# Kernel tuning notes

Measured on AMD Instinct MI355X. Metric: run time of the kernel, lower is better.

Reference implementation:

```python
import jax, jax.numpy as jnp
import numpy as np

NUM_HEADS = 16

def setup_inputs() -> dict:
    key = jax.random.key(0)
    ks = jax.random.split(key, 7)
    B, Q, K, D = 4, 512, 4096, 1024
    return {
        'query':  jax.random.normal(ks[0], (B, Q, D), dtype=jnp.float32),
        'memory': jax.random.normal(ks[1], (B, K, D), dtype=jnp.float32),
        'bias':   jax.random.normal(ks[2], (B, K), dtype=jnp.float32),
        'Wq': jax.random.normal(ks[3], (D, D), dtype=jnp.float32) * (D ** -0.5),
        'Wk': jax.random.normal(ks[4], (D, D), dtype=jnp.float32) * (D ** -0.5),
        'Wv': jax.random.normal(ks[5], (D, D), dtype=jnp.float32) * (D ** -0.5),
        'Wo': jax.random.normal(ks[6], (D, D), dtype=jnp.float32) * (D ** -0.5),
    }

def reference(query, memory, bias, Wq, Wk, Wv, Wo):
    B, Qn, _ = query.shape
    _, Kn, _ = memory.shape
    H = NUM_HEADS
    E = Wq.shape[1]
    dh = E // H
    scale = dh ** -0.5
    # projections (bias-free linears), split heads: [B, H, len, dh]
    q = (query @ Wq).reshape(B, Qn, H, dh).transpose(0, 2, 1, 3)
    k = (memory @ Wk).reshape(B, Kn, H, dh).transpose(0, 2, 1, 3)
    v = (memory @ Wv).reshape(B, Kn, H, dh).transpose(0, 2, 1, 3)
    scores = jnp.einsum('bhqd,bhkd->bhqk', q, k) * scale
    scores = scores + bias[:, None, None, :]          # additive support bias over K
    weights = jax.nn.softmax(scores, axis=-1)          # dropout p=0.0 -> identity
    out = jnp.einsum('bhqk,bhkd->bhqd', weights, v)
    out = out.transpose(0, 2, 1, 3).reshape(B, Qn, E)
    return out @ Wo
```

## Files before the change

kernel.cpp:

```cpp
#include <hip/hip_runtime.h>

typedef __attribute__((ext_vector_type(8))) short bf16x8;
typedef __attribute__((ext_vector_type(4))) short bf16x4;
typedef __attribute__((ext_vector_type(4))) float f32x4;

#define MFMA32(a,b,c) __builtin_amdgcn_mfma_f32_16x16x32_bf16((a),(b),(c),0,0,0)
#define MFMA16(a,b,c) __builtin_amdgcn_mfma_f32_16x16x16bf16_1k((a),(b),(c),0,0,0)
#define LOG2E 1.44269504f

#define BAR() asm volatile("s_barrier" ::: "memory")
#define VMW(n) asm volatile("s_waitcnt vmcnt(" #n ")" ::: "memory")

__device__ __forceinline__ unsigned short f2bf(float f) {
  unsigned int u = __float_as_uint(f);
  u += 0x7fffu + ((u >> 16) & 1u);
  return (unsigned short)(u >> 16);
}

__device__ __forceinline__ void cp16(const void* g, void* l) {
  __builtin_amdgcn_global_load_lds((const __attribute__((address_space(1))) void*)g,
                                   (__attribute__((address_space(3))) void*)l, 16, 0, 0);
}

__global__ void conv_both(const float* __restrict__ q, const float* __restrict__ m,
                          const float* __restrict__ bias,
                          unsigned short* __restrict__ qo, unsigned short* __restrict__ mo,
                          float* __restrict__ bz) {
  int i = blockIdx.x * 256 + threadIdx.x;
  if (i < 524288) {
    float4 v = ((const float4*)q)[i];
    ushort4 o; o.x = f2bf(v.x); o.y = f2bf(v.y); o.z = f2bf(v.z); o.w = f2bf(v.w);
    ((ushort4*)qo)[i] = o;
  } else if (i < 4718592) {
    int j = i - 524288;
    float4 v = ((const float4*)m)[j];
    ushort4 o; o.x = f2bf(v.x); o.y = f2bf(v.y); o.z = f2bf(v.z); o.w = f2bf(v.w);
    ((ushort4*)mo)[j] = o;
  } else {
    int j = i - 4718592;
    float4 v = ((const float4*)bias)[j];
    float4 o;
    o.x = __builtin_fmaf(v.x, LOG2E, -16.f);
    o.y = __builtin_fmaf(v.y, LOG2E, -16.f);
    o.z = __builtin_fmaf(v.z, LOG2E, -16.f);
    o.w = __builtin_fmaf(v.w, LOG2E, -16.f);
    ((float4*)bz)[j] = o;
  }
}

__global__ void transpose4(const float* __restrict__ Wq, const float* __restrict__ Wk,
                           const float* __restrict__ Wv, const float* __restrict__ Wo,
                           unsigned short* __restrict__ dst) {
  __shared__ float t[32][33];
  int z = blockIdx.z;
  const float* W = (z == 0) ? Wq : (z == 1) ? Wk : (z == 2) ? Wv : Wo;
  unsigned short* WT = dst + (size_t)z * 1048576;
  int bx = blockIdx.x * 32, by = blockIdx.y * 32;
  int x = threadIdx.x, y0 = threadIdx.y;
#pragma unroll
  for (int r = 0; r < 4; ++r)
    t[y0 + r * 8][x] = W[(size_t)(by + y0 + r * 8) * 1024 + bx + x];
  __syncthreads();
#pragma unroll
  for (int r = 0; r < 4; ++r)
    WT[(size_t)(bx + y0 + r * 8) * 1024 + by + x] = f2bf(t[x][y0 + r * 8]);
}

__global__ __launch_bounds__(512, 2) void gemm_kv(
    const unsigned short* __restrict__ A,
    const unsigned short* __restrict__ Bk,
    const unsigned short* __restrict__ Bv,
    unsigned short* __restrict__ Kp,
    unsigned short* __restrict__ Vt)
{
  __shared__ __attribute__((aligned(16))) unsigned short lds[65536];
  const int tid = threadIdx.x;
  const int w = tid >> 6, lane = tid & 63;
  const int lh = lane & 15, q4 = lane >> 4;
  const int id = blockIdx.x;
  const int xcd = id & 7, j = id >> 3;
  const int tm = (xcd * 8 + (j >> 3)) * 256;
  const int tn = (j & 7) * 128;
  const int wm = (w >> 1) * 64, wn = (w & 1) * 64;

  const int r8 = lane >> 3;
  const int scol = ((lane & 7) ^ r8) * 8;
  const int srow = w * 8 + r8;
  const int fs0 = ((0 + q4) ^ (lh & 7)) * 8;
  const int fs1 = ((4 + q4) ^ (lh & 7)) * 8;

  const unsigned short* Ag = A  + (size_t)tm * 1024 + scol;
  const unsigned short* Kg = Bk + (size_t)tn * 1024 + scol;
  const unsigned short* Vg = Bv + (size_t)tn * 1024 + scol;

#define STG_A(BUF,KT,I) cp16(Ag + (size_t)((I)*64 + srow) * 1024 + (KT)*64, \
                             lds + (BUF)*32768 + (I)*4096 + w*512)
#define STG_K(BUF,KT,I) cp16(Kg + (size_t)((I)*64 + srow) * 1024 + (KT)*64, \
                             lds + (BUF)*32768 + 16384 + (I)*4096 + w*512)
#define STG_V(BUF,KT,I) cp16(Vg + (size_t)((I)*64 + srow) * 1024 + (KT)*64, \
                             lds + (BUF)*32768 + 24576 + (I)*4096 + w*512)

  f32x4 acck[4][4] = {}, accv[4][4] = {};

  STG_A(0, 0, 0); STG_A(0, 0, 1); STG_A(0, 0, 2); STG_A(0, 0, 3);
  STG_K(0, 0, 0); STG_K(0, 0, 1);
  STG_V(0, 0, 0); STG_V(0, 0, 1);
  STG_A(1, 1, 0); STG_A(1, 1, 1); STG_A(1, 1, 2); STG_A(1, 1, 3);
  VMW(6);
  BAR();

#define KV_TILE(CURB, TP1, TP2, DO_SB, DO_SA, VM1N, DO_V3, VM3N)              \
  {                                                                           \
    const unsigned short* bse = lds + (CURB) * 32768;                         \
    const int nx = (CURB) ^ 1;                                                \
    bf16x8 a0[4], a1[4], bfr[4];                                              \
                                                  \
    _Pragma("unroll") for (int m = 0; m < 4; ++m)                             \
      a0[m] = *(const bf16x8*)(bse + (wm + m * 16 + lh) * 64 + fs0);          \
    _Pragma("unroll") for (int n = 0; n < 4; ++n)                             \
      bfr[n] = *(const bf16x8*)(bse + 16384 + (wn + n * 16 + lh) * 64 + fs0); \
    if (DO_SB) { STG_K(nx, TP1, 0); STG_K(nx, TP1, 1); }                      \
    BAR();                                                                    \
    __builtin_amdgcn_s_setprio(1);                                            \
    _Pragma("unroll") for (int m = 0; m < 4; ++m)                             \
      _Pragma("unroll") for (int n = 0; n < 4; ++n)                           \
        acck[m][n] = MFMA32(a0[m], bfr[n], acck[m][n]);                       \
    __builtin_amdgcn_s_setprio(0);                                            \
    BAR();                                                                    \
                                                  \
    _Pragma("unroll") for (int m = 0; m < 4; ++m)                             \
      a1[m] = *(const bf16x8*)(bse + (wm + m * 16 + lh) * 64 + fs1);          \
    _Pragma("unroll") for (int n = 0; n < 4; ++n)                             \
      bfr[n] = *(const bf16x8*)(bse + 16384 + (wn + n * 16 + lh) * 64 + fs1); \
    if (DO_SB) { STG_V(nx, TP1, 0); STG_V(nx, TP1, 1); }                      \
    BAR();                                                                    \
    __builtin_amdgcn_s_setprio(1);                                            \
    _Pragma("unroll") for (int m = 0; m < 4; ++m)                             \
      _Pragma("unroll") for (int n = 0; n < 4; ++n)                           \
        acck[m][n] = MFMA32(a1[m], bfr[n], acck[m][n]);                       \
    __builtin_amdgcn_s_setprio(0);                                            \
    VMW(VM1N);                                                                \
    BAR();                                                                    \
                                  \
    _Pragma("unroll") for (int n = 0; n < 4; ++n)                             \
      bfr[n] = *(const bf16x8*)(bse + 24576 + (wn + n * 16 + lh) * 64 + fs0); \
    if (DO_SA) { STG_A(CURB, TP2, 0); STG_A(CURB, TP2, 1); }                  \
    BAR();                                                                    \
    __builtin_amdgcn_s_setprio(1);                                            \
    _Pragma("unroll") for (int m = 0; m < 4; ++m)                             \
      _Pragma("unroll") for (int n = 0; n < 4; ++n)                           \
        accv[m][n] = MFMA32(a0[m], bfr[n], accv[m][n]);                       \
    __builtin_amdgcn_s_setprio(0);                                            \
    BAR();                                                                    \
                                                  \
    _Pragma("unroll") for (int n = 0; n < 4; ++n)                             \
      bfr[n] = *(const bf16x8*)(bse + 24576 + (wn + n * 16 + lh) * 64 + fs1); \
    if (DO_SA) { STG_A(CURB, TP2, 2); STG_A(CURB, TP2, 3); }                  \
    BAR();                                                                    \
    __builtin_amdgcn_s_setprio(1);                                            \
    _Pragma("unroll") for (int m = 0; m < 4; ++m)                             \
      _Pragma("unroll") for (int n = 0; n < 4; ++n)                           \
        accv[m][n] = MFMA32(a1[m], bfr[n], accv[m][n]);                       \
    __builtin_amdgcn_s_setprio(0);                                            \
    if (DO_V3) { VMW(VM3N); }                                                 \
    BAR();                                                                    \
  }

  for (int t = 0; t < 14; ++t) {
    KV_TILE(t & 1, t + 1, t + 2, 1, 1, 8, 1, 6);
  }
  KV_TILE(0, 15, 16, 1, 0, 8, 1, 2);
  KV_TILE(1, 16, 17, 0, 0, 0, 0, 0);

#undef KV_TILE
#undef STG_A
#undef STG_K
#undef STG_V

#pragma unroll
  for (int m = 0; m < 4; ++m)
#pragma unroll
    for (int n = 0; n < 4; ++n) {
      int row = tm + wm + m * 16 + q4 * 4;
      int col = tn + wn + n * 16 + lh;
#pragma unroll
      for (int e = 0; e < 4; ++e)
        Kp[(size_t)(row + e) * 1024 + col] = f2bf(acck[m][n][e]);
    }

#pragma unroll
  for (int m = 0; m < 4; ++m)
#pragma unroll
    for (int n = 0; n < 4; ++n) {
      int row = wm + m * 16 + q4 * 4;
      int col = wn + n * 16 + lh;
      ushort4 v4;
      v4.x = f2bf(accv[m][n][0]); v4.y = f2bf(accv[m][n][1]);
      v4.z = f2bf(accv[m][n][2]); v4.w = f2bf(accv[m][n][3]);
      *(ushort4*)(lds + col * 256 + (row ^ ((col & 31) << 3))) = v4;
    }
  __syncthreads();
#pragma unroll
  for (int p = 0; p < 8; ++p) {
    int col = p * 16 + (tid >> 5);
    int jb = tid & 31;
    const unsigned short* src = lds + col * 256 + ((jb ^ (col & 31)) << 3);
    *(int4*)(Vt + (size_t)(tn + col) * 16384 + tm + jb * 8) = *(const int4*)src;
  }
}

__global__ __launch_bounds__(256) void gemm_bt64(
    const unsigned short* __restrict__ A, const unsigned short* __restrict__ B,
    float* __restrict__ Cf, unsigned short* __restrict__ Cb,
    int M, int N, int K, float scale)
{
  __shared__ __attribute__((aligned(16))) unsigned short lds[6144];
  int w = threadIdx.x >> 6, lane = threadIdx.x & 63;
  int lh = lane & 15, q4 = lane >> 4;
  int tm = blockIdx.y * 128, tn = blockIdx.x * 64;
  int wm = (w & 1) * 64, wn = (w >> 1) * 32;

  int srow = lane >> 2;
  int scol = ((lane & 3) ^ ((lane >> 3) & 3)) << 3;
  int q4s = (q4 ^ ((lh >> 1) & 3)) << 3;

  f32x4 acc[4][2] = {};

  for (int k0 = 0; k0 < K; k0 += 32) {
#pragma unroll
    for (int i = 0; i < 2; ++i) {
      int c = w * 2 + i;
      int row = c * 16 + srow;
      cp16(A + (size_t)(tm + row) * K + k0 + scol, lds + c * 512);
    }
    {
      int row = w * 16 + srow;
      cp16(B + (size_t)(tn + row) * K + k0 + scol, lds + 4096 + w * 512);
    }
    __syncthreads();
    bf16x8 afr[4], bfr[2];
#pragma unroll
    for (int r = 0; r < 4; ++r)
      afr[r] = *(const bf16x8*)(lds + (wm + r * 16 + lh) * 32 + q4s);
#pragma unroll
    for (int c = 0; c < 2; ++c)
      bfr[c] = *(const bf16x8*)(lds + 4096 + (wn + c * 16 + lh) * 32 + q4s);
#pragma unroll
    for (int r = 0; r < 4; ++r)
#pragma unroll
      for (int c = 0; c < 2; ++c)
        acc[r][c] = MFMA32(afr[r], bfr[c], acc[r][c]);
    __syncthreads();
  }

#pragma unroll
  for (int r = 0; r < 4; ++r)
#pragma unroll
    for (int c = 0; c < 2; ++c)
#pragma unroll
      for (int e = 0; e < 4; ++e) {
        int row = tm + wm + r * 16 + q4 * 4 + e;
        int col = tn + wn + c * 16 + lh;
        if (Cb) Cb[(size_t)row * N + col] = f2bf(acc[r][c][e] * scale);
        else    Cf[(size_t)row * N + col] = acc[r][c][e] * scale;
      }
}

__global__ __launch_bounds__(256) void attn_kernel(
    const unsigned short* __restrict__ Q, const unsigned short* __restrict__ Kp,
    const unsigned short* __restrict__ VT, const float* __restrict__ bz,
    float* __restrict__ po, float* __restrict__ lp)
{
  __shared__ __attribute__((aligned(16))) unsigned short Klds[4096];
  __shared__ __attribute__((aligned(16))) unsigned short Vlds[4096];
  int w = threadIdx.x >> 6, lane = threadIdx.x & 63;
  int lh = lane & 15, q4 = lane >> 4;

  int id = blockIdx.x;
  int xcd = id & 7, j = id >> 3;
  int ql = j & 7;
  int half = ql & 1, qt = ql >> 1;
  int bh = (j >> 3) * 8 + xcd;
  int b = bh >> 4, h = bh & 15;
  int q0 = qt * 128;
  int t00 = half * 2048;

  const unsigned short* Qb = Q + (size_t)(b * 512 + q0 + w * 32) * 1024 + h * 64;
  const unsigned short* Kb = Kp + (size_t)(b * 4096) * 1024 + h * 64;
  const unsigned short* Vb = VT + (size_t)(h * 64) * 16384 + b * 4096;
  const float* bzg = bz + (size_t)b * 4096;

  bf16x8 bq[2][2];
#pragma unroll
  for (int s = 0; s < 2; ++s)
#pragma unroll
    for (int th = 0; th < 2; ++th)
      bq[s][th] = *(const bf16x8*)(Qb + (size_t)(s * 16 + lh) * 1024 + th * 32 + q4 * 8);

  f32x4 oa[2][4] = {};
  float ls[2] = {0.f, 0.f};

  int rl = lane >> 3, blk = lane & 7;
  int sw = ((blk ^ rl) * 8);

  for (int ti = 0; ti < 32; ++ti) {
    int t = t00 + ti * 64;
#pragma unroll
    for (int r = 0; r < 2; ++r) {
      int seg = r * 4 + w;
      int row = seg * 8 + rl;
      cp16(Kb + (size_t)(t + row) * 1024 + sw, Klds + seg * 512);
      cp16(Vb + (size_t)row * 16384 + t + sw, Vlds + seg * 512);
    }
    __syncthreads();

    float4 bz4[4];
#pragma unroll
    for (int c = 0; c < 4; ++c)
      bz4[c] = *(const float4*)(bzg + t + c * 16 + q4 * 4);

    bf16x8 kf[4][2];
#pragma unroll
    for (int c = 0; c < 4; ++c)
#pragma unroll
      for (int th = 0; th < 2; ++th)
        kf[c][th] = *(const bf16x8*)(Klds + (c * 16 + lh) * 64 + (((th << 2) + q4) ^ (lh & 7)) * 8);
    bf16x4 vf[4][4];
#pragma unroll
    for (int c = 0; c < 4; ++c)
#pragma unroll
      for (int c2 = 0; c2 < 4; ++c2)
        vf[c][c2] = *(const bf16x4*)(Vlds + (c2 * 16 + lh) * 64 +
                                     (((c << 1) + (q4 >> 1)) ^ (lh & 7)) * 8 + (q4 & 1) * 4);

#pragma unroll
    for (int s = 0; s < 2; ++s) {
#pragma unroll
      for (int c = 0; c < 4; ++c) {
        f32x4 z = {};
        z = MFMA32(kf[c][0], bq[s][0], z);
        z = MFMA32(kf[c][1], bq[s][1], z);
        float bzf[4] = {bz4[c].x, bz4[c].y, bz4[c].z, bz4[c].w};
        bf16x4 pb;
        float ps = 0.f;
#pragma unroll
        for (int e = 0; e < 4; ++e) {
          float p = __builtin_amdgcn_exp2f(z[e] + bzf[e]);
          ps += p;
          pb[e] = (short)f2bf(p);
        }
        ls[s] += ps;
#pragma unroll
        for (int c2 = 0; c2 < 4; ++c2)
          oa[s][c2] = MFMA16(vf[c][c2], pb, oa[s][c2]);
      }
    }
    __syncthreads();
  }

#pragma unroll
  for (int s = 0; s < 2; ++s) {
    ls[s] += __shfl_xor(ls[s], 16);
    ls[s] += __shfl_xor(ls[s], 32);
  }

  int sl = bh * 4 + qt;
  float* pslice = po + (size_t)(half * 256 + sl) * 8192;
#pragma unroll
  for (int s = 0; s < 2; ++s) {
    if (q4 == 0) lp[half * 32768 + sl * 128 + w * 32 + s * 16 + lh] = ls[s];
#pragma unroll
    for (int c2 = 0; c2 < 4; ++c2)
#pragma unroll
      for (int e = 0; e < 4; ++e)
        pslice[(c2 * 16 + q4 * 4 + e) * 128 + w * 32 + s * 16 + lh] = oa[s][c2][e];
  }
}

__global__ void norm_kernel(const float* __restrict__ po, const float* __restrict__ lp,
                            unsigned short* __restrict__ ao) {
  int g = blockIdx.x * 256 + threadIdx.x;
  int d8 = (g & 7) * 8;
  int rowid = g >> 3;
  int bh = rowid >> 9, rq = rowid & 511, qt = rq >> 7, qcol = rq & 127;
  int sl = bh * 4 + qt;
  const float* p0 = po + (size_t)sl * 8192;
  const float* p1 = po + (size_t)(256 + sl) * 8192;
  float l = lp[sl * 128 + qcol] + lp[32768 + sl * 128 + qcol];
  float inv = 1.f / l;
  unsigned short o8[8];
#pragma unroll
  for (int k = 0; k < 8; ++k)
    o8[k] = f2bf((p0[(d8 + k) * 128 + qcol] + p1[(d8 + k) * 128 + qcol]) * inv);
  int b = bh >> 4, h = bh & 15;
  unsigned short* dst = ao + (size_t)(b * 512 + qt * 128 + qcol) * 1024 + h * 64 + d8;
  *(ushort4*)dst = *(ushort4*)o8;
  *(ushort4*)(dst + 4) = *(ushort4*)(o8 + 4);
}

extern "C" void kernel_launch(void* const* d_in, const int* in_sizes, int n_in,
                              void* d_out, int out_size, void* d_ws, size_t ws_size,
                              hipStream_t stream) {
  const float* query  = (const float*)d_in[0];
  const float* memory = (const float*)d_in[1];
  const float* bias   = (const float*)d_in[2];
  const float* Wq     = (const float*)d_in[3];
  const float* Wk     = (const float*)d_in[4];
  const float* Wv     = (const float*)d_in[5];
  const float* Wo     = (const float*)d_in[6];
  float* out = (float*)d_out;

  unsigned short* ws  = (unsigned short*)d_ws;
  unsigned short* qbf = ws;
  unsigned short* mbf = qbf + 2097152;
  unsigned short* WqT = mbf + 16777216;
  unsigned short* WkT = WqT + 1048576;
  unsigned short* WvT = WkT + 1048576;
  unsigned short* WoT = WvT + 1048576;
  unsigned short* qp  = WoT + 1048576;
  unsigned short* kp  = qp + 2097152;
  unsigned short* vT  = kp + 16777216;
  unsigned short* ao  = vT + 16777216;
  float* bzw = (float*)(ao + 2097152);
  float* po = (float*)ws;
  float* lp = po + 4194304;

  conv_both<<<18448, 256, 0, stream>>>(query, memory, bias, qbf, mbf, bzw);
  transpose4<<<dim3(32, 32, 4), dim3(32, 8), 0, stream>>>(Wq, Wk, Wv, Wo, WqT);

  gemm_bt64<<<dim3(16, 16), 256, 0, stream>>>(qbf, WqT, nullptr, qp, 2048, 1024, 1024, 0.125f * LOG2E);
  gemm_kv<<<512, 512, 0, stream>>>(mbf, WkT, WvT, kp, vT);

  attn_kernel<<<512, 256, 0, stream>>>(qp, kp, vT, bzw, po, lp);
  norm_kernel<<<1024, 256, 0, stream>>>(po, lp, ao);

  gemm_bt64<<<dim3(16, 16), 256, 0, stream>>>(ao, WoT, out, nullptr, 2048, 1024, 1024, 1.f);
}
```

Measured before the change: 299.3 us.

## Software-pipeline LDS fragment reads with double-buffered registers in KV projection

Restructures the K/V projection tile loop so LDS fragment reads for the next phase (and the next tile's first A/K fragments) are issued before the current MFMA block, using separate register sets instead of reloading each phase. Barriers drop from two per phase to one, and the vmcnt wait thresholds are retuned to fit the new ordering. The aim is to hide LDS read latency behind MFMA work and cut barrier stalls. In exchange it raises register pressure and makes the barrier and wait ordering more fragile, so a read could race with an async LDS fill if a count is wrong. A __syncthreads is added before the V tile is staged into LDS for the transpose.

```diff
diff --git a/kernel.cpp b/kernel.cpp
--- a/kernel.cpp
+++ b/kernel.cpp
@@ -9,7 +9,8 @@
 #define LOG2E 1.44269504f
 
 #define BAR() asm volatile("s_barrier" ::: "memory")
-#define VMW(n) asm volatile("s_waitcnt vmcnt(" #n ")" ::: "memory")
+#define VMW_(n) asm volatile("s_waitcnt vmcnt(" #n ")" ::: "memory")
+#define VMW(n) VMW_(n)
 
 __device__ __forceinline__ unsigned short f2bf(float f) {
   unsigned int u = __float_as_uint(f);
@@ -101,6 +102,7 @@
                              lds + (BUF)*32768 + 24576 + (I)*4096 + w*512)
 
   f32x4 acck[4][4] = {}, accv[4][4] = {};
+  bf16x8 aE[4], aO[4], bP[4], bQ[4];
 
   STG_A(0, 0, 0); STG_A(0, 0, 1); STG_A(0, 0, 2); STG_A(0, 0, 3);
   STG_K(0, 0, 0); STG_K(0, 0, 1);
@@ -108,69 +110,73 @@
   STG_A(1, 1, 0); STG_A(1, 1, 1); STG_A(1, 1, 2); STG_A(1, 1, 3);
   VMW(6);
   BAR();
-
-#define KV_TILE(CURB, TP1, TP2, DO_SB, DO_SA, VM1N, DO_V3, VM3N)              \
+#pragma unroll
+  for (int m = 0; m < 4; ++m)
+    aE[m] = *(const bf16x8*)(lds + (wm + m * 16 + lh) * 64 + fs0);
+#pragma unroll
+  for (int n = 0; n < 4; ++n)
+    bP[n] = *(const bf16x8*)(lds + 16384 + (wn + n * 16 + lh) * 64 + fs0);
+
+#define KV_TILE(CURB, TP1, TP2, DO_SB, DO_SA, VM1N, VM3N, DO_V3, DO_RDN)      \
   {                                                                           \
     const unsigned short* bse = lds + (CURB) * 32768;                         \
+    const unsigned short* bnx = lds + ((CURB) ^ 1) * 32768;                   \
     const int nx = (CURB) ^ 1;                                                \
-    bf16x8 a0[4], a1[4], bfr[4];                                              \
-                                                  \
+                            \
+    BAR();                                                                    \
     _Pragma("unroll") for (int m = 0; m < 4; ++m)                             \
-      a0[m] = *(const bf16x8*)(bse + (wm + m * 16 + lh) * 64 + fs0);          \
+      aO[m] = *(const bf16x8*)(bse + (wm + m * 16 + lh) * 64 + fs1);          \
     _Pragma("unroll") for (int n = 0; n < 4; ++n)                             \
-      bfr[n] = *(const bf16x8*)(bse + 16384 + (wn + n * 16 + lh) * 64 + fs0); \
+      bQ[n] = *(const bf16x8*)(bse + 16384 + (wn + n * 16 + lh) * 64 + fs1);  \
     if (DO_SB) { STG_K(nx, TP1, 0); STG_K(nx, TP1, 1); }                      \
-    BAR();                                                                    \
     __builtin_amdgcn_s_setprio(1);                                            \
     _Pragma("unroll") for (int m = 0; m < 4; ++m)                             \
       _Pragma("unroll") for (int n = 0; n < 4; ++n)                           \
-        acck[m][n] = MFMA32(a0[m], bfr[n], acck[m][n]);                       \
+        acck[m][n] = MFMA32(aE[m], bP[n], acck[m][n]);                        \
     __builtin_amdgcn_s_setprio(0);                                            \
+                      \
+    VMW(VM1N);                                                                \
     BAR();                                                                    \
-                                                  \
-    _Pragma("unroll") for (int m = 0; m < 4; ++m)                             \
-      a1[m] = *(const bf16x8*)(bse + (wm + m * 16 + lh) * 64 + fs1);          \
     _Pragma("unroll") for (int n = 0; n < 4; ++n)                             \
-      bfr[n] = *(const bf16x8*)(bse + 16384 + (wn + n * 16 + lh) * 64 + fs1); \
+      bP[n] = *(const bf16x8*)(bse + 24576 + (wn + n * 16 + lh) * 64 + fs0);  \
     if (DO_SB) { STG_V(nx, TP1, 0); STG_V(nx, TP1, 1); }                      \
-    BAR();                                                                    \
     __builtin_amdgcn_s_setprio(1);                                            \
     _Pragma("unroll") for (int m = 0; m < 4; ++m)                             \
       _Pragma("unroll") for (int n = 0; n < 4; ++n)                           \
-        acck[m][n] = MFMA32(a1[m], bfr[n], acck[m][n]);                       \
+        acck[m][n] = MFMA32(aO[m], bQ[n], acck[m][n]);                        \
     __builtin_amdgcn_s_setprio(0);                                            \
-    VMW(VM1N);                                                                \
+                         \
     BAR();                                                                    \
-                                  \
     _Pragma("unroll") for (int n = 0; n < 4; ++n)                             \
-      bfr[n] = *(const bf16x8*)(bse + 24576 + (wn + n * 16 + lh) * 64 + fs0); \
+      bQ[n] = *(const bf16x8*)(bse + 24576 + (wn + n * 16 + lh) * 64 + fs1);  \
     if (DO_SA) { STG_A(CURB, TP2, 0); STG_A(CURB, TP2, 1); }                  \
-    BAR();                                                                    \
     __builtin_amdgcn_s_setprio(1);                                            \
     _Pragma("unroll") for (int m = 0; m < 4; ++m)                             \
       _Pragma("unroll") for (int n = 0; n < 4; ++n)                           \
-        accv[m][n] = MFMA32(a0[m], bfr[n], accv[m][n]);                       \
+        accv[m][n] = MFMA32(aE[m], bP[n], accv[m][n]);                        \
     __builtin_amdgcn_s_setprio(0);                                            \
+                   \
+    if (DO_V3) { VMW(VM3N); }                                                 \
     BAR();                                                                    \
-                                                  \
-    _Pragma("unroll") for (int n = 0; n < 4; ++n)                             \
-      bfr[n] = *(const bf16x8*)(bse + 24576 + (wn + n * 16 + lh) * 64 + fs1); \
+    if (DO_RDN) {                                                             \
+      _Pragma("unroll") for (int m = 0; m < 4; ++m)                           \
+        aE[m] = *(const bf16x8*)(bnx + (wm + m * 16 + lh) * 64 + fs0);        \
+      _Pragma("unroll") for (int n = 0; n < 4; ++n)                           \
+        bP[n] = *(const bf16x8*)(bnx + 16384 + (wn + n * 16 + lh) * 64 + fs0);\
+    }                                                                         \
     if (DO_SA) { STG_A(CURB, TP2, 2); STG_A(CURB, TP2, 3); }                  \
-    BAR();                                                                    \
     __builtin_amdgcn_s_setprio(1);                                            \
     _Pragma("unroll") for (int m = 0; m < 4; ++m)                             \
       _Pragma("unroll") for (int n = 0; n < 4; ++n)                           \
-        accv[m][n] = MFMA32(a1[m], bfr[n], accv[m][n]);                       \
+        accv[m][n] = MFMA32(aO[m], bQ[n], accv[m][n]);                        \
     __builtin_amdgcn_s_setprio(0);                                            \
-    if (DO_V3) { VMW(VM3N); }                                                 \
-    BAR();                                                                    \
   }
 
   for (int t = 0; t < 14; ++t) {
-    KV_TILE(t & 1, t + 1, t + 2, 1, 1, 8, 1, 6);
-  }
-  KV_TILE(0, 15, 16, 1, 0, 8, 1, 2);
-  KV_TILE(1, 16, 17, 0, 0, 0, 0, 0);
+    KV_TILE(t & 1, t + 1, t + 2, 1, 1, 6, 4, 1, 1);
+  }
+  KV_TILE(0, 15, 16, 1, 0, 6, 2, 1, 1);
+  KV_TILE(1, 16, 17, 0, 0, 0, 0, 0, 0);
 
 #undef KV_TILE
 #undef STG_A
@@ -188,6 +194,7 @@
         Kp[(size_t)(row + e) * 1024 + col] = f2bf(acck[m][n][e]);
     }
 
+  __syncthreads();
 #pragma unroll
   for (int m = 0; m < 4; ++m)
 #pragma unroll
```

New measurement: 304.4 us. About the same (+1.7%).
